# Performance work log

Measured on AMD Instinct MI355X. Metric: run time of the kernel, lower is better.

Reference implementation:

```python
import jax, jax.numpy as jnp
import numpy as np

B, S, D, H = 4, 2048, 1024, 16
DH = D // H
NEG = -1.0e9


def setup_inputs() -> dict:
    key = jax.random.key(0)
    ks = jax.random.split(key, 12)
    sc = 1.0 / np.sqrt(D)
    inp = {
        'q': jax.random.normal(ks[0], (B, S, D), jnp.float32),
        'k': jax.random.normal(ks[1], (B, S, D), jnp.float32),
        'v': jax.random.normal(ks[2], (B, S, D), jnp.float32),
        # causal mask: 1.0 where attention is disallowed (strictly upper triangular)
        'mask': jnp.triu(jnp.ones((S, S), jnp.float32), k=1)[None, None, :, :],
        'Wq': jax.random.normal(ks[3], (D, D), jnp.float32) * sc,
        'bq': jnp.zeros((D,), jnp.float32),
        'Wk': jax.random.normal(ks[4], (D, D), jnp.float32) * sc,
        'bk': jnp.zeros((D,), jnp.float32),
        'Wv': jax.random.normal(ks[5], (D, D), jnp.float32) * sc,
        'bv': jnp.zeros((D,), jnp.float32),
        'Wo': jax.random.normal(ks[6], (D, D), jnp.float32) * sc,
        'bo': jnp.zeros((D,), jnp.float32),
    }
    return inp


def _split_heads(x):
    # [B,S,D] -> [B,H,S,DH]
    return x.reshape(B, S, H, DH).transpose(0, 2, 1, 3)


def reference(q, k, v, mask, Wq, bq, Wk, bk, Wv, bv, Wo, bo):
    _q = _split_heads(q @ Wq.T + bq)
    _k = _split_heads(k @ Wk.T + bk)
    _v = _split_heads(v @ Wv.T + bv)
    # faithful quirk: mask*-1e9 added BEFORE scaling, scale = sqrt(model_dim)
    score = jnp.einsum('bhqd,bhkd->bhqk', _q, _k) + mask * NEG
    attn = jax.nn.softmax(score / jnp.sqrt(jnp.float32(D)), axis=-1)
    ctx = jnp.einsum('bhqk,bhkd->bhqd', attn, _v)
    ctx = ctx.transpose(0, 2, 1, 3).reshape(B, S, D)
    return ctx @ Wo.T + bo
```

## Files before the change

kernel.cpp:

```cpp
#include <hip/hip_runtime.h>
#include <hip/hip_bf16.h>

#define S_ 2048
#define DH_ 64
#define NE_ 8388608

using f32x4  = __attribute__((ext_vector_type(4))) float;
using bf16x8 = __attribute__((ext_vector_type(8))) __bf16;
using bf16x4 = __attribute__((ext_vector_type(4))) __bf16;

__device__ __forceinline__ unsigned int f2bf(float f) {
    union { float f; unsigned int u; } x; x.f = f;
    return (x.u + 0x7FFFu + ((x.u >> 16) & 1u)) >> 16;
}

__device__ __forceinline__ void gl_lds16(const unsigned short* g, unsigned short* l) {
    __builtin_amdgcn_global_load_lds(
        (const __attribute__((address_space(1))) unsigned int*)(const void*)g,
        (__attribute__((address_space(3))) unsigned int*)(void*)l,
        16, 0, 0);
}

__global__ __launch_bounds__(256) void cvt_all(const float* __restrict__ w0, const float* __restrict__ w1,
                                               const float* __restrict__ w2, const float* __restrict__ w3,
                                               const float* __restrict__ a0, const float* __restrict__ a1,
                                               const float* __restrict__ a2,
                                               unsigned short* __restrict__ wout,
                                               unsigned short* __restrict__ aout) {
    const int y = blockIdx.y;
    const float* src;
    unsigned short* dst;
    if (y < 4) {
        if (blockIdx.x >= 1024) return;
        src = y == 0 ? w0 : y == 1 ? w1 : y == 2 ? w2 : w3;
        dst = wout + (size_t)y * 1048576;
    } else {
        src = y == 4 ? a0 : y == 5 ? a1 : a2;
        dst = aout + (size_t)(y - 4) * NE_;
    }
    int i = (blockIdx.x * 256 + threadIdx.x) * 4;
    float4 v = *(const float4*)&src[i];
    ushort4 h;
    h.x = f2bf(v.x); h.y = f2bf(v.y); h.z = f2bf(v.z); h.w = f2bf(v.w);
    *(ushort4*)&dst[i] = h;
}

template<int OMODE>
__global__ __launch_bounds__(512, 2) void gemm2ph(const unsigned short* __restrict__ Aact,
                                                  const unsigned short* __restrict__ Bw,
                                                  const float* __restrict__ bq,
                                                  const float* __restrict__ bk,
                                                  const float* __restrict__ bvv,
                                                  unsigned short* __restrict__ Qp,
                                                  unsigned short* __restrict__ Kp,
                                                  unsigned short* __restrict__ VTp,
                                                  float* __restrict__ Cf,
                                                  float scq)
{
    __shared__ unsigned short lds[49152];
    unsigned short* ldsA = lds;
    unsigned short* ldsB = lds + 32768;

    const int q8 = gridDim.x >> 3;
    const int lid = (blockIdx.x & 7) * q8 + (blockIdx.x >> 3);
    const int bx = lid & 31;
    const int by = lid >> 5;

    const unsigned short* Ag = (OMODE == 0) ? Aact + (size_t)(by >> 3) * NE_ : Aact;
    const int arow0 = bx * 256;
    const int brow0 = by * 128;

    const int tid = threadIdx.x, lane = tid & 63, wid = tid >> 6;
    const int fr = lane & 15, fg = lane >> 4;
    const int wid_m = wid >> 1, wid_n = wid & 1;

    const int srcRow0 = wid * 16 + (lane >> 3);
    const int scolS = ((lane & 7) ^ ((lane >> 3) & 7)) << 3;

    auto STG = [&](int ldsOff, const unsigned short* g, int grow, int kk) {
        const unsigned short* s0 = g + (size_t)(grow + srcRow0) * 1024 + kk + scolS;
        gl_lds16(s0, lds + ldsOff + wid * 1024 + lane * 8);
        gl_lds16(s0 + 8 * 1024, lds + ldsOff + wid * 1024 + 512 + lane * 8);
    };

    const int fx = fr & 7;
    const int vA0 = wid_m * 4096 + fr * 64 + ((fg ^ fx) << 3);
    const int vA1 = wid_m * 4096 + fr * 64 + (((4 | fg) ^ fx) << 3);
    const int vB0 = wid_n * 4096 + fr * 64 + ((fg ^ fx) << 3);
    const int vB1 = wid_n * 4096 + fr * 64 + (((4 | fg) ^ fx) << 3);

    f32x4 acc[4][4] = {};

    STG(0,            Ag, arow0,       0);
    STG(8192,         Ag, arow0 + 128, 0);
    STG(32768,        Bw, brow0,       0);
    STG(32768 + 8192, Bw, brow0,      64);
    asm volatile("s_waitcnt vmcnt(2)" ::: "memory");
    __builtin_amdgcn_s_barrier();

    for (int t = 0; t < 16; ++t) {
        const int cur = t & 1;
        const int ldA = cur * 16384, ldB = cur * 8192;

        bf16x8 bfr[4][2], af[2][2];
        #pragma unroll
        for (int j = 0; j < 4; ++j) {
            bfr[j][0] = *(const bf16x8*)&ldsB[ldB + vB0 + j * 1024];
            bfr[j][1] = *(const bf16x8*)&ldsB[ldB + vB1 + j * 1024];
        }
        #pragma unroll
        for (int i = 0; i < 2; ++i) {
            af[i][0] = *(const bf16x8*)&ldsA[ldA + vA0 + i * 1024];
            af[i][1] = *(const bf16x8*)&ldsA[ldA + vA1 + i * 1024];
        }
        {
            const int ka = ((t + 1) & 15) * 64;
            STG((cur ^ 1) * 16384,        Ag, arow0,       ka);
            STG((cur ^ 1) * 16384 + 8192, Ag, arow0 + 128, ka);
        }
        __builtin_amdgcn_s_barrier();
        asm volatile("s_waitcnt lgkmcnt(0)" ::: "memory");
        __builtin_amdgcn_s_setprio(1);
        #pragma unroll
        for (int i = 0; i < 2; ++i)
            #pragma unroll
            for (int j = 0; j < 4; ++j) {
                acc[i][j] = __builtin_amdgcn_mfma_f32_16x16x32_bf16(af[i][0], bfr[j][0], acc[i][j], 0, 0, 0);
                acc[i][j] = __builtin_amdgcn_mfma_f32_16x16x32_bf16(af[i][1], bfr[j][1], acc[i][j], 0, 0, 0);
            }
        __builtin_amdgcn_s_setprio(0);
        __builtin_amdgcn_s_barrier();

        bf16x8 af2[2][2];
        #pragma unroll
        for (int i = 0; i < 2; ++i) {
            af2[i][0] = *(const bf16x8*)&ldsA[ldA + vA0 + (2 + i) * 1024];
            af2[i][1] = *(const bf16x8*)&ldsA[ldA + vA1 + (2 + i) * 1024];
        }
        {
            const int kb = ((t + 2) & 15) * 64;
            STG(32768 + ldB, Bw, brow0, kb);
        }
        asm volatile("s_waitcnt vmcnt(2)" ::: "memory");
        __builtin_amdgcn_s_barrier();
        asm volatile("s_waitcnt lgkmcnt(0)" ::: "memory");
        __builtin_amdgcn_s_setprio(1);
        #pragma unroll
        for (int i = 0; i < 2; ++i)
            #pragma unroll
            for (int j = 0; j < 4; ++j) {
                acc[2 + i][j] = __builtin_amdgcn_mfma_f32_16x16x32_bf16(af2[i][0], bfr[j][0], acc[2 + i][j], 0, 0, 0);
                acc[2 + i][j] = __builtin_amdgcn_mfma_f32_16x16x32_bf16(af2[i][1], bfr[j][1], acc[2 + i][j], 0, 0, 0);
            }
        __builtin_amdgcn_s_setprio(0);
        __builtin_amdgcn_s_barrier();
    }
    asm volatile("s_waitcnt vmcnt(0)" ::: "memory");

    const int row00 = bx * 256 + wid_m * 64;
    if (OMODE == 1) {
        const int col0 = by * 128 + wid_n * 64;
        #pragma unroll
        for (int i = 0; i < 4; ++i)
            #pragma unroll
            for (int j = 0; j < 4; ++j) {
                int c = col0 + j * 16 + fr;
                float bv = bq[c];
                #pragma unroll
                for (int r = 0; r < 4; ++r) {
                    int row = row00 + i * 16 + fg * 4 + r;
                    Cf[(size_t)row * 1024 + c] = acc[i][j][r] + bv;
                }
            }
    } else {
        const int range = by >> 3;
        const float os = range == 0 ? scq : 1.0f;
        const float* bp = range == 0 ? bq : range == 1 ? bk : bvv;
        unsigned short* OP = range == 0 ? Qp : Kp;
        const int colbase = (by & 7) * 128 + wid_n * 64;
        #pragma unroll
        for (int i = 0; i < 4; ++i)
            #pragma unroll
            for (int j = 0; j < 4; ++j) {
                int colr = colbase + j * 16 + fr;
                float bias = bp[colr];
                int h = colr >> 6, dh = colr & 63;
                if (range == 2) {
                    int row = row00 + i * 16 + fg * 4;
                    int b = row >> 11, s = row & 2047;
                    unsigned int w0 = f2bf(acc[i][j][0] + bias) | (f2bf(acc[i][j][1] + bias) << 16);
                    unsigned int w1 = f2bf(acc[i][j][2] + bias) | (f2bf(acc[i][j][3] + bias) << 16);
                    *(uint2*)&VTp[((size_t)((b << 4) + h) * 64 + dh) * 2048 + s] = make_uint2(w0, w1);
                } else {
                    #pragma unroll
                    for (int r = 0; r < 4; ++r) {
                        int row = row00 + i * 16 + fg * 4 + r;
                        int b = row >> 11, s = row & 2047;
                        OP[((((b << 4) + h) * 2048 + s) << 6) + dh] =
                            (unsigned short)f2bf((acc[i][j][r] + bias) * os);
                    }
                }
            }
    }
}

__global__ __launch_bounds__(512, 4) void attn_fwd5(const unsigned short* __restrict__ Qp,
                                                    const unsigned short* __restrict__ Kp,
                                                    const unsigned short* __restrict__ VTg,
                                                    unsigned short* __restrict__ ctx)
{
    __shared__ unsigned short Ks[64][68];
    __shared__ unsigned short Vt[64][68];
    __shared__ unsigned short Ps[8][16][68];

    const int lin = blockIdx.x;
    const int xcd = lin & 7;
    const int w = lin >> 3;
    const int bh = xcd * 8 + (w & 7);
    const int j = 15 - (w >> 3);
    const int b = bh >> 4, h = bh & 15;
    const int tid = threadIdx.x, lane = tid & 63, wid = tid >> 6;
    const int fr = lane & 15, fg = lane >> 4;

    const unsigned short* Qh  = Qp  + (size_t)bh * (S_ * DH_);
    const unsigned short* Kh  = Kp  + (size_t)bh * (S_ * DH_);
    const unsigned short* VTh = VTg + (size_t)bh * (DH_ * S_);

    const int srow = tid >> 3;
    const int scol = (tid & 7) * 8;

    bf16x8 ones;
    #pragma unroll
    for (int i = 0; i < 8; ++i) ones[i] = (__bf16)1.0f;

    const int q0 = j * 128;
    const int ntiles = 2 * (j + 1);
    const int rbase = q0 + wid * 16;
    const int qg = rbase + fr;

    bf16x8 qf[2];
    #pragma unroll
    for (int ks = 0; ks < 2; ++ks)
        qf[ks] = *(const bf16x8*)&Qh[(size_t)qg * 64 + ks * 32 + 8 * fg];

    f32x4 oacc[4] = {};
    float m_run = -3.0e38f, l_run = 0.0f;

    int4 kreg = *(const int4*)&Kh[(size_t)srow * 64 + scol];
    int4 vreg = *(const int4*)&VTh[(size_t)srow * 2048 + scol];

    for (int kt = 0; kt < ntiles; ++kt) {
        const int kv0 = kt * 64;
        __syncthreads();
        *(int4*)&Ks[srow][scol] = kreg;
        *(int4*)&Vt[srow][scol] = vreg;
        if (kt + 1 < ntiles) {
            const int kv1 = kv0 + 64;
            kreg = *(const int4*)&Kh[(size_t)(kv1 + srow) * 64 + scol];
            vreg = *(const int4*)&VTh[(size_t)srow * 2048 + kv1 + scol];
        }
        __syncthreads();

        if (kv0 > rbase + 15) continue;

        f32x4 sacc[4] = {};
        #pragma unroll
        for (int nt = 0; nt < 4; ++nt)
            #pragma unroll
            for (int ks = 0; ks < 2; ++ks) {
                bf16x8 kf = *(const bf16x8*)&Ks[nt * 16 + fr][ks * 32 + 8 * fg];
                sacc[nt] = __builtin_amdgcn_mfma_f32_16x16x32_bf16(kf, qf[ks], sacc[nt], 0, 0, 0);
            }

        if (kv0 + 63 > rbase) {
            const int kbase = kv0 + fg * 4;
            #pragma unroll
            for (int nt = 0; nt < 4; ++nt)
                #pragma unroll
                for (int r = 0; r < 4; ++r)
                    if (kbase + nt * 16 + r > qg) sacc[nt][r] = -3.0e38f;
        }

        float vm = sacc[0][0];
        #pragma unroll
        for (int nt = 0; nt < 4; ++nt)
            #pragma unroll
            for (int r = 0; r < 4; ++r) vm = fmaxf(vm, sacc[nt][r]);
        vm = fmaxf(vm, __shfl_xor(vm, 16));
        vm = fmaxf(vm, __shfl_xor(vm, 32));

        if (!__all(vm - m_run <= 8.0f)) {
            const float mn = fmaxf(m_run, vm);
            const float alpha = exp2f(m_run - mn);
            m_run = mn;
            l_run *= alpha;
            #pragma unroll
            for (int dt = 0; dt < 4; ++dt)
                #pragma unroll
                for (int r = 0; r < 4; ++r) oacc[dt][r] *= alpha;
        }

        #pragma unroll
        for (int nt = 0; nt < 4; ++nt) {
            bf16x4 t;
            t[0] = (__bf16)exp2f(sacc[nt][0] - m_run);
            t[1] = (__bf16)exp2f(sacc[nt][1] - m_run);
            t[2] = (__bf16)exp2f(sacc[nt][2] - m_run);
            t[3] = (__bf16)exp2f(sacc[nt][3] - m_run);
            *(bf16x4*)&Ps[wid][fr][nt * 16 + fg * 4] = t;
        }
        asm volatile("s_waitcnt lgkmcnt(0)" ::: "memory");

        bf16x8 pb[2];
        #pragma unroll
        for (int ks = 0; ks < 2; ++ks)
            pb[ks] = *(const bf16x8*)&Ps[wid][fr][ks * 32 + 8 * fg];

        f32x4 racc = {};
        #pragma unroll
        for (int ks = 0; ks < 2; ++ks)
            racc = __builtin_amdgcn_mfma_f32_16x16x32_bf16(ones, pb[ks], racc, 0, 0, 0);
        #pragma unroll
        for (int dt = 0; dt < 4; ++dt)
            #pragma unroll
            for (int ks = 0; ks < 2; ++ks) {
                bf16x8 vf = *(const bf16x8*)&Vt[dt * 16 + fr][ks * 32 + 8 * fg];
                oacc[dt] = __builtin_amdgcn_mfma_f32_16x16x32_bf16(vf, pb[ks], oacc[dt], 0, 0, 0);
            }
        l_run += racc[0];
    }

    const float linv = 1.0f / l_run;
    unsigned short* cb = &ctx[(size_t)(b * 2048 + qg) * 1024 + h * 64];
    #pragma unroll
    for (int dt = 0; dt < 4; ++dt) {
        unsigned int w0 = f2bf(oacc[dt][0] * linv) | (f2bf(oacc[dt][1] * linv) << 16);
        unsigned int w1 = f2bf(oacc[dt][2] * linv) | (f2bf(oacc[dt][3] * linv) << 16);
        *(uint2*)&cb[dt * 16 + fg * 4] = make_uint2(w0, w1);
    }
}

extern "C" void kernel_launch(void* const* d_in, const int* in_sizes, int n_in,
                              void* d_out, int out_size, void* d_ws, size_t ws_size,
                              hipStream_t stream)
{
    const float* q  = (const float*)d_in[0];
    const float* k  = (const float*)d_in[1];
    const float* v  = (const float*)d_in[2];
    const float* Wq = (const float*)d_in[4];
    const float* bq = (const float*)d_in[5];
    const float* Wk = (const float*)d_in[6];
    const float* bk = (const float*)d_in[7];
    const float* Wv = (const float*)d_in[8];
    const float* bv = (const float*)d_in[9];
    const float* Wo = (const float*)d_in[10];
    const float* bo = (const float*)d_in[11];
    float* out = (float*)d_out;

    unsigned short* Wcat = (unsigned short*)d_ws;
    unsigned short* actb = Wcat + 4 * 1048576;
    unsigned short* Qp   = actb + 3 * (size_t)NE_;
    unsigned short* Kp   = Qp + NE_;
    unsigned short* VTp  = Kp + NE_;
    unsigned short* Ctx  = VTp + NE_;

    const float SCQ = 0.045084220027780106f;

    dim3 blk(256);
    cvt_all<<<dim3(8192, 7), blk, 0, stream>>>(Wq, Wk, Wv, Wo, q, k, v, Wcat, actb);

    gemm2ph<0><<<dim3(768), dim3(512), 0, stream>>>(actb, Wcat, bq, bk, bv,
                                                    Qp, Kp, VTp, nullptr, SCQ);

    attn_fwd5<<<dim3(1024), dim3(512), 0, stream>>>(Qp, Kp, VTp, Ctx);

    gemm2ph<1><<<dim3(256), dim3(512), 0, stream>>>(Ctx, Wcat + 3 * 1048576, bo,
                                                    nullptr, nullptr, nullptr, nullptr,
                                                    nullptr, out, 1.0f);
}
```

Baseline: 212.5 us.

## Use 256x256 tiles for QKV projection GEMM and reorder attention block scheduling

The QKV projection GEMM moves from 256x128 tiles on 768 blocks to 256x256 tiles on 384 blocks. It uses 128KB of LDS, eight accumulator rows per wave, and a restructured K-loop that spreads global-to-LDS staging across four sub-steps. The aim is to raise arithmetic intensity and cut redundant A-tile loads, at the cost of heavy register and LDS pressure, which may stop two blocks from fitting per CU. The attention kernel also reorders its block-to-query-tile mapping into a zigzag pattern, so causal work per CU is better balanced across waves of blocks.

```diff
diff --git a/kernel.cpp b/kernel.cpp
--- a/kernel.cpp
+++ b/kernel.cpp
@@ -45,17 +45,141 @@
     *(ushort4*)&dst[i] = h;
 }
 
-template<int OMODE>
-__global__ __launch_bounds__(512, 2) void gemm2ph(const unsigned short* __restrict__ Aact,
+__global__ __launch_bounds__(512, 2) void gemm_qkv8(const unsigned short* __restrict__ actb,
+                                                    const unsigned short* __restrict__ Wcat,
+                                                    const float* __restrict__ bq,
+                                                    const float* __restrict__ bk,
+                                                    const float* __restrict__ bvv,
+                                                    unsigned short* __restrict__ Qp,
+                                                    unsigned short* __restrict__ Kp,
+                                                    unsigned short* __restrict__ VTp,
+                                                    float scq)
+{
+    __shared__ unsigned short lds[65536];
+    unsigned short* ldsA = lds;
+    unsigned short* ldsB = lds + 32768;
+
+    const int orig = blockIdx.x;
+    const int lid = (orig & 7) * 48 + (orig >> 3);
+    const int bx = lid & 31;
+    const int by = lid >> 5;
+    const int range = by >> 2;
+    const unsigned short* Aact = actb + (size_t)range * NE_;
+
+    const int tid = threadIdx.x, lane = tid & 63, wid = tid >> 6;
+    const int fr = lane & 15, fg = lane >> 4;
+    const int wid_m = wid >> 2, wid_n = wid & 3;
+
+    const int srcRow0 = wid * 16 + (lane >> 3);
+    const int scolS = ((lane & 7) ^ ((lane >> 3) & 7)) << 3;
+
+    auto STG = [&](int ldsRegion, const unsigned short* g, int grow, int kk) {
+        const unsigned short* s0 = g + (size_t)(grow + srcRow0) * 1024 + kk + scolS;
+        gl_lds16(s0, lds + ldsRegion + wid * 1024 + lane * 8);
+        gl_lds16(s0 + 8 * 1024, lds + ldsRegion + wid * 1024 + 512 + lane * 8);
+    };
+
+    const int fx = fr & 7;
+    const int vA0 = wid_m * 8192 + fr * 64 + ((fg ^ fx) << 3);
+    const int vA1 = wid_m * 8192 + fr * 64 + (((4 | fg) ^ fx) << 3);
+    const int vBr = (wid_n & 1) * 4096 + (wid_n >> 1) * 8192 + fr * 64;
+    const int vB0 = vBr + ((fg ^ fx) << 3);
+    const int vB1 = vBr + (((4 | fg) ^ fx) << 3);
+
+    f32x4 acc[8][4] = {};
+    bf16x8 bfr[4][2];
+
+    STG(0,          Aact, bx * 256,       0);
+    STG(8192,       Aact, bx * 256 + 128, 0);
+    STG(32768,      Wcat, by * 256,       0);
+    STG(32768+8192, Wcat, by * 256 + 128, 0);
+    STG(32768+16384,       Wcat, by * 256,       64);
+    STG(32768+16384+8192,  Wcat, by * 256 + 128,  64);
+    asm volatile("s_waitcnt vmcnt(4)" ::: "memory");
+    __builtin_amdgcn_s_barrier();
+
+#define KTILE(BUF, ABUF, TA, BBUF, TB)                                              \
+  {                                                                                 \
+    _Pragma("unroll")                                                               \
+    for (int q = 0; q < 4; ++q) {                                                   \
+      if (q == 0) {                                                                 \
+        _Pragma("unroll")                                                           \
+        for (int j = 0; j < 4; ++j) {                                               \
+          bfr[j][0] = *(const bf16x8*)&ldsB[(BUF)*16384 + vB0 + j*1024];            \
+          bfr[j][1] = *(const bf16x8*)&ldsB[(BUF)*16384 + vB1 + j*1024];            \
+        }                                                                           \
+      }                                                                             \
+      bf16x8 af[2][2];                                                              \
+      _Pragma("unroll")                                                             \
+      for (int i2 = 0; i2 < 2; ++i2) {                                              \
+        af[i2][0] = *(const bf16x8*)&ldsA[(BUF)*16384 + vA0 + (q*2+i2)*1024];       \
+        af[i2][1] = *(const bf16x8*)&ldsA[(BUF)*16384 + vA1 + (q*2+i2)*1024];       \
+      }                                                                             \
+      if (q == 0) STG((ABUF)*16384,        Aact, bx*256,       ((TA)&15)*64);       \
+      if (q == 1) STG((ABUF)*16384 + 8192, Aact, bx*256 + 128, ((TA)&15)*64);       \
+      if (q == 2) STG(32768 + (BBUF)*16384,        Wcat, by*256,       ((TB)&15)*64); \
+      if (q == 3) { STG(32768 + (BBUF)*16384 + 8192, Wcat, by*256 + 128, ((TB)&15)*64); \
+                    asm volatile("s_waitcnt vmcnt(4)" ::: "memory"); }              \
+      __builtin_amdgcn_s_barrier();                                                 \
+      asm volatile("s_waitcnt lgkmcnt(0)" ::: "memory");                            \
+      __builtin_amdgcn_s_setprio(1);                                                \
+      _Pragma("unroll")                                                             \
+      for (int i2 = 0; i2 < 2; ++i2)                                                \
+        _Pragma("unroll")                                                           \
+        for (int j = 0; j < 4; ++j) {                                               \
+          acc[q*2+i2][j] = __builtin_amdgcn_mfma_f32_16x16x32_bf16(af[i2][0], bfr[j][0], acc[q*2+i2][j], 0, 0, 0); \
+          acc[q*2+i2][j] = __builtin_amdgcn_mfma_f32_16x16x32_bf16(af[i2][1], bfr[j][1], acc[q*2+i2][j], 0, 0, 0); \
+        }                                                                           \
+      __builtin_amdgcn_s_setprio(0);                                                \
+      __builtin_amdgcn_s_barrier();                                                 \
+    }                                                                               \
+  }
+
+    for (int it = 0; it < 8; ++it) {
+        const int t0 = 2 * it;
+        KTILE(0, 1, t0 + 1, 0, t0 + 2);
+        KTILE(1, 0, t0 + 2, 1, t0 + 3);
+    }
+#undef KTILE
+
+    asm volatile("s_waitcnt vmcnt(0)" ::: "memory");
+
+    const float* bp = range == 0 ? bq : range == 1 ? bk : bvv;
+    const float os = range == 0 ? scq : 1.0f;
+    unsigned short* OP = range == 0 ? Qp : Kp;
+    const int row00 = bx * 256 + wid_m * 128;
+    const int col0r = (by & 3) * 256 + wid_n * 64;
+
+    #pragma unroll
+    for (int i = 0; i < 8; ++i) {
+        #pragma unroll
+        for (int j = 0; j < 4; ++j) {
+            int colr = col0r + j * 16 + fr;
+            float bias = bp[colr];
+            int h = colr >> 6, dh = colr & 63;
+            if (range == 2) {
+                int row = row00 + i * 16 + fg * 4;
+                int b = row >> 11, s = row & 2047;
+                unsigned int w0 = f2bf(acc[i][j][0] + bias) | (f2bf(acc[i][j][1] + bias) << 16);
+                unsigned int w1 = f2bf(acc[i][j][2] + bias) | (f2bf(acc[i][j][3] + bias) << 16);
+                *(uint2*)&VTp[((size_t)((b << 4) + h) * 64 + dh) * 2048 + s] = make_uint2(w0, w1);
+            } else {
+                #pragma unroll
+                for (int r = 0; r < 4; ++r) {
+                    int row = row00 + i * 16 + fg * 4 + r;
+                    int b = row >> 11, s = row & 2047;
+                    OP[((((b << 4) + h) * 2048 + s) << 6) + dh] =
+                        (unsigned short)f2bf((acc[i][j][r] + bias) * os);
+                }
+            }
+        }
+    }
+}
+
+__global__ __launch_bounds__(512, 2) void gemm_o2(const unsigned short* __restrict__ Aact,
                                                   const unsigned short* __restrict__ Bw,
-                                                  const float* __restrict__ bq,
-                                                  const float* __restrict__ bk,
-                                                  const float* __restrict__ bvv,
-                                                  unsigned short* __restrict__ Qp,
-                                                  unsigned short* __restrict__ Kp,
-                                                  unsigned short* __restrict__ VTp,
-                                                  float* __restrict__ Cf,
-                                                  float scq)
+                                                  const float* __restrict__ bias,
+                                                  float* __restrict__ Cf)
 {
     __shared__ unsigned short lds[49152];
     unsigned short* ldsA = lds;
@@ -66,7 +190,6 @@
     const int bx = lid & 31;
     const int by = lid >> 5;
 
-    const unsigned short* Ag = (OMODE == 0) ? Aact + (size_t)(by >> 3) * NE_ : Aact;
     const int arow0 = bx * 256;
     const int brow0 = by * 128;
 
@@ -91,8 +214,8 @@
 
     f32x4 acc[4][4] = {};
 
-    STG(0,            Ag, arow0,       0);
-    STG(8192,         Ag, arow0 + 128, 0);
+    STG(0,            Aact, arow0,       0);
+    STG(8192,         Aact, arow0 + 128, 0);
     STG(32768,        Bw, brow0,       0);
     STG(32768 + 8192, Bw, brow0,      64);
     asm volatile("s_waitcnt vmcnt(2)" ::: "memory");
@@ -115,8 +238,8 @@
         }
         {
             const int ka = ((t + 1) & 15) * 64;
-            STG((cur ^ 1) * 16384,        Ag, arow0,       ka);
-            STG((cur ^ 1) * 16384 + 8192, Ag, arow0 + 128, ka);
+            STG((cur ^ 1) * 16384,        Aact, arow0,       ka);
+            STG((cur ^ 1) * 16384 + 8192, Aact, arow0 + 128, ka);
         }
         __builtin_amdgcn_s_barrier();
         asm volatile("s_waitcnt lgkmcnt(0)" ::: "memory");
@@ -158,56 +281,25 @@
     asm volatile("s_waitcnt vmcnt(0)" ::: "memory");
 
     const int row00 = bx * 256 + wid_m * 64;
-    if (OMODE == 1) {
-        const int col0 = by * 128 + wid_n * 64;
-        #pragma unroll
-        for (int i = 0; i < 4; ++i)
-            #pragma unroll
-            for (int j = 0; j < 4; ++j) {
-                int c = col0 + j * 16 + fr;
-                float bv = bq[c];
-                #pragma unroll
-                for (int r = 0; r < 4; ++r) {
-                    int row = row00 + i * 16 + fg * 4 + r;
-                    Cf[(size_t)row * 1024 + c] = acc[i][j][r] + bv;
-                }
-            }
-    } else {
-        const int range = by >> 3;
-        const float os = range == 0 ? scq : 1.0f;
-        const float* bp = range == 0 ? bq : range == 1 ? bk : bvv;
-        unsigned short* OP = range == 0 ? Qp : Kp;
-        const int colbase = (by & 7) * 128 + wid_n * 64;
-        #pragma unroll
-        for (int i = 0; i < 4; ++i)
-            #pragma unroll
-            for (int j = 0; j < 4; ++j) {
-                int colr = colbase + j * 16 + fr;
-                float bias = bp[colr];
-                int h = colr >> 6, dh = colr & 63;
-                if (range == 2) {
-                    int row = row00 + i * 16 + fg * 4;
-                    int b = row >> 11, s = row & 2047;
-                    unsigned int w0 = f2bf(acc[i][j][0] + bias) | (f2bf(acc[i][j][1] + bias) << 16);
-                    unsigned int w1 = f2bf(acc[i][j][2] + bias) | (f2bf(acc[i][j][3] + bias) << 16);
-                    *(uint2*)&VTp[((size_t)((b << 4) + h) * 64 + dh) * 2048 + s] = make_uint2(w0, w1);
-                } else {
-                    #pragma unroll
-                    for (int r = 0; r < 4; ++r) {
-                        int row = row00 + i * 16 + fg * 4 + r;
-                        int b = row >> 11, s = row & 2047;
-                        OP[((((b << 4) + h) * 2048 + s) << 6) + dh] =
-                            (unsigned short)f2bf((acc[i][j][r] + bias) * os);
-                    }
-                }
-            }
-    }
-}
-
-__global__ __launch_bounds__(512, 4) void attn_fwd5(const unsigned short* __restrict__ Qp,
-                                                    const unsigned short* __restrict__ Kp,
-                                                    const unsigned short* __restrict__ VTg,
-                                                    unsigned short* __restrict__ ctx)
+    const int col0 = by * 128 + wid_n * 64;
+    #pragma unroll
+    for (int i = 0; i < 4; ++i)
+        #pragma unroll
+        for (int j = 0; j < 4; ++j) {
+            int c = col0 + j * 16 + fr;
+            float bv = bias[c];
+            #pragma unroll
+            for (int r = 0; r < 4; ++r) {
+                int row = row00 + i * 16 + fg * 4 + r;
+                Cf[(size_t)row * 1024 + c] = acc[i][j][r] + bv;
+            }
+        }
+}
+
+__global__ __launch_bounds__(512, 4) void attn_fwd5b(const unsigned short* __restrict__ Qp,
+                                                     const unsigned short* __restrict__ Kp,
+                                                     const unsigned short* __restrict__ VTg,
+                                                     unsigned short* __restrict__ ctx)
 {
     __shared__ unsigned short Ks[64][68];
     __shared__ unsigned short Vt[64][68];
@@ -216,8 +308,11 @@
     const int lin = blockIdx.x;
     const int xcd = lin & 7;
     const int w = lin >> 3;
-    const int bh = xcd * 8 + (w & 7);
-    const int j = 15 - (w >> 3);
+    const int k = w >> 5;
+    const int c = w & 31;
+    const int s = c >> 3;
+    const int bh = xcd * 8 + (c & 7);
+    const int j = (k == 0) ? 15 - s : (k == 1) ? 8 + s : (k == 2) ? 7 - s : s;
     const int b = bh >> 4, h = bh & 15;
     const int tid = threadIdx.x, lane = tid & 63, wid = tid >> 6;
     const int fr = lane & 15, fg = lane >> 4;
@@ -369,12 +464,9 @@
     dim3 blk(256);
     cvt_all<<<dim3(8192, 7), blk, 0, stream>>>(Wq, Wk, Wv, Wo, q, k, v, Wcat, actb);
 
-    gemm2ph<0><<<dim3(768), dim3(512), 0, stream>>>(actb, Wcat, bq, bk, bv,
-                                                    Qp, Kp, VTp, nullptr, SCQ);
-
-    attn_fwd5<<<dim3(1024), dim3(512), 0, stream>>>(Qp, Kp, VTp, Ctx);
-
-    gemm2ph<1><<<dim3(256), dim3(512), 0, stream>>>(Ctx, Wcat + 3 * 1048576, bo,
-                                                    nullptr, nullptr, nullptr, nullptr,
-                                                    nullptr, out, 1.0f);
-}
+    gemm_qkv8<<<dim3(384), dim3(512), 0, stream>>>(actb, Wcat, bq, bk, bv, Qp, Kp, VTp, SCQ);
+
+    attn_fwd5b<<<dim3(1024), dim3(512), 0, stream>>>(Qp, Kp, VTp, Ctx);
+
+    gemm_o2<<<dim3(256), dim3(512), 0, stream>>>(Ctx, Wcat + 3 * 1048576, bo, out);
+}
```

Result: faster. 204.0 us (-4.0%).
